# Kernel optimization log

Measured on AMD Instinct MI355X. Metric: run time of the kernel, lower is better.

The kernel has to match this reference:

```python
import jax, jax.numpy as jnp
import numpy as np

LMAX = 2
C1 = 64; C2 = 64; COUT = 64
B = 4096
SUM_RDIM = sum(3**L for L in range(LMAX + 1))   # 13
FEAT1 = C1 * SUM_RDIM                            # 832
FEAT2 = C2 * SUM_RDIM


def _enumerate_paths(Lmax):
    paths = []
    for L1 in range(Lmax + 1):
        for L2 in range(Lmax + 1):
            for k in range(min(L1, L2) + 1):
                Lout = L1 + L2 - 2 * k
                if 0 <= Lout <= Lmax:
                    paths.append((L1, L2, Lout, k, False))
            if L1 >= 1 and L2 >= 1:
                for k in range(min(L1 - 1, L2 - 1) + 1):
                    Lout = L1 + L2 - 2 * k - 1
                    if 0 <= Lout <= Lmax:
                        paths.append((L1, L2, Lout, k, True))
    return paths

PATHS = _enumerate_paths(LMAX)   # 15 paths for Lmax=2


def _path_eq(L1, L2, k, use_eps):
    # Fused equation: W[c,a,b] contracted together with the delta/eps path einsum.
    letters = list('defghijklmnopqrstuvwxyz')  # a,b,c reserved for channels
    i_idx = letters[:L1]
    j_idx = letters[L1:L1 + L2]
    for r in range(k):  # delta: contract last k indices of A with last k of B
        j_idx[L2 - k + r] = i_idx[L1 - k + r]
    i_free = i_idx[:L1 - k]
    j_free = j_idx[:L2 - k]
    eps_sub = None
    if use_eps:  # consume last free index of each side via eps_{p i j}
        p = letters[L1 + L2]
        eps_sub = p + i_free[-1] + j_free[-1]
        i_free, j_free = i_free[:-1], j_free[:-1]
        out = i_free + j_free + [p]
    else:
        out = i_free + j_free
    terms = ['cab', '...a' + ''.join(i_idx), '...b' + ''.join(j_idx)]
    if eps_sub is not None:
        terms.append(eps_sub)
    return ','.join(terms) + '->...c' + ''.join(out)


def _epsilon():
    e = np.zeros((3, 3, 3), dtype=np.float32)
    e[0, 1, 2] = e[1, 2, 0] = e[2, 0, 1] = 1.0
    e[2, 1, 0] = e[1, 0, 2] = e[0, 2, 1] = -1.0
    return jnp.asarray(e)


def _split_by_rank(x, C, Lmax):
    batch = x.shape[:-1]
    out, idx = {}, 0
    for L in range(Lmax + 1):
        d = C * 3**L
        blk = x[..., idx:idx + d]
        idx += d
        out[L] = blk.reshape(*batch, C) if L == 0 else blk.reshape(*batch, C, *((3,) * L))
    return out


def setup_inputs() -> dict:
    key = jax.random.key(0)
    k1, k2, k3 = jax.random.split(key, 3)
    x1 = jax.random.normal(k1, (B, FEAT1), dtype=jnp.float32)
    x2 = jax.random.normal(k2, (B, FEAT2), dtype=jnp.float32)
    weight = jax.random.normal(k3, (len(PATHS) * COUT * C1 * C2,), dtype=jnp.float32) * 0.02
    return {"x1": x1, "x2": x2, "weight": weight}


def reference(x1, x2, weight):
    A = _split_by_rank(x1, C1, LMAX)
    Bt = _split_by_rank(x2, C2, LMAX)
    eps = _epsilon().astype(x1.dtype)
    batch = x1.shape[:-1]
    blocks = {L: jnp.zeros((*batch, COUT) + (3,) * L, dtype=x1.dtype) for L in range(LMAX + 1)}
    wsz = COUT * C1 * C2
    for n, (L1, L2, Lout, k, use_eps) in enumerate(PATHS):
        Wp = weight[n * wsz:(n + 1) * wsz].reshape(COUT, C1, C2)
        eq = _path_eq(L1, L2, k, use_eps)
        ops = (Wp, A[L1], Bt[L2]) + ((eps,) if use_eps else ())
        blocks[Lout] = blocks[Lout] + jnp.einsum(eq, *ops, optimize='optimal')
    parts = [blocks[L].reshape(*batch, COUT * 3**L) for L in range(LMAX + 1)]
    return jnp.concatenate(parts, axis=-1)
```

## Files before the change

kernel.cpp:

```cpp
#include <hip/hip_runtime.h>
#include <cstdint>
#include <cstddef>


#define FEAT 832
#define ZT 64

typedef _Float16 half8 __attribute__((ext_vector_type(8)));
typedef float floatx16 __attribute__((ext_vector_type(16)));

struct Chunk {
  int wbase;
  int o1[3];
  int o2[3];
  float sg[3];
  int d1, d2, nt;
};

__global__ void swz_w_kernel(const float* __restrict__ w, _Float16* __restrict__ o) {
  const int i = blockIdx.x * 256 + threadIdx.x;
  const int lane = i & 63;
  const int pkc  = i >> 6;
  const int cgrp = pkc & 1;
  const int ksg  = (pkc >> 1) & 255;
  const int p    = pkc >> 9;
  const int c  = cgrp * 32 + (lane & 31);
  const int k0 = ksg * 16 + (lane >> 5) * 8;
  const float* src = w + (size_t)p * 262144 + (size_t)c * 4096 + k0;
  const float4 v0 = *(const float4*)(src);
  const float4 v1 = *(const float4*)(src + 4);
  half8 h = { (_Float16)v0.x, (_Float16)v0.y, (_Float16)v0.z, (_Float16)v0.w,
              (_Float16)v1.x, (_Float16)v1.y, (_Float16)v1.z, (_Float16)v1.w };
  *(half8*)(o + (size_t)i * 8) = h;
}

__global__ __launch_bounds__(256) void gather_kernel(
    float* __restrict__ out, const float* __restrict__ part)
{
  __shared__ float T[64][65];
  const int zb = blockIdx.x * 64;
  const int fb = blockIdx.y * 64;
  const int tid = threadIdx.x;
  const int fl = tid >> 6;
  const int zl = tid & 63;
  #pragma unroll
  for (int i = 0; i < 16; ++i) {
    const int f = fb + fl + i * 4;
    int s, c;
    if (f < 64)       { s = 0;              c = f; }
    else if (f < 256) { const int g = f - 64;  c = g / 3; s = 1 + g % 3; }
    else              { const int g = f - 256; c = g / 9; s = 4 + g % 9; }
    T[fl + i * 4][zl] = part[(size_t)s * 262144 + (size_t)c * 4096 + zb + zl];
  }
  __syncthreads();
  const int zr = tid >> 6;
  const int fc = tid & 63;
  #pragma unroll
  for (int i = 0; i < 16; ++i) {
    const int z = zr + i * 4;
    float* o = out + (size_t)(zb + z) * FEAT + fb + fc;
    *o += T[fc][z];
  }
}

__device__ __forceinline__ half8 splat8(_Float16 h) {
  return half8{h, h, h, h, h, h, h, h};
}

template<int NT>
__device__ __forceinline__ void run_chunk(
    const Chunk C, const int zbase, const int zl, const int hf,
    const int lane, const int tid,
    const float* __restrict__ x1, const float* __restrict__ x2,
    const _Float16* __restrict__ Wh, _Float16* __restrict__ XS,
    floatx16& acc0, floatx16& acc1)
{
  __syncthreads();

  #pragma unroll
  for (int t = 0; t < NT; ++t) {
    const size_t base2 = (size_t)zbase * FEAT + C.o2[t];
    for (int e = tid; e < 4096; e += 128) {
      const int zz = e >> 6, b = e & 63;
      XS[(t * 64 + zz) * 72 + b] =
          (_Float16)x2[base2 + (size_t)zz * FEAT + b * C.d2];
    }
  }
  __syncthreads();

  half8 x2r[NT][4];
  #pragma unroll
  for (int t = 0; t < NT; ++t) {
    #pragma unroll
    for (int ks = 0; ks < 4; ++ks)
      x2r[t][ks] = *(const half8*)&XS[(t * 64 + zl) * 72 + ks * 16 + hf * 8];
  }
  __syncthreads();

  #pragma unroll
  for (int t = 0; t < NT; ++t) {
    const float sgf = C.sg[t];
    const int o1 = C.o1[t];
    for (int e = tid; e < 4096; e += 128) {
      const int a = e & 63, zz = e >> 6;
      XS[(t * 64 + a) * 66 + zz] =
          (_Float16)(x1[(size_t)(zbase + zz) * FEAT + o1 + a * C.d1] * sgf);
    }
  }
  __syncthreads();

  const _Float16* __restrict__ Wq = Wh + C.wbase + lane * 8;
  const _Float16* __restrict__ Xq = XS + zl;

  half8 afE[2][4], afO[2][4];
  #pragma unroll
  for (int ks = 0; ks < 4; ++ks) {
    afE[0][ks] = *(const half8*)(Wq + ks * 1024);
    afE[1][ks] = *(const half8*)(Wq + ks * 1024 + 512);
    afO[0][ks] = *(const half8*)(Wq + 4096 + ks * 1024);
    afO[1][ks] = *(const half8*)(Wq + 4096 + ks * 1024 + 512);
  }
  _Float16 sc[NT], scn[NT];
  #pragma unroll
  for (int t = 0; t < NT; ++t) {
    sc[t]  = Xq[(t * 64 + 0) * 66];
    scn[t] = Xq[(t * 64 + 1) * 66];
  }

  #pragma unroll 1
  for (int a = 0; a < 64; a += 2) {
    {
      half8 sv[NT];
      #pragma unroll
      for (int t = 0; t < NT; ++t) sv[t] = splat8(sc[t]);
      if (a + 2 < 64) {
        #pragma unroll
        for (int t = 0; t < NT; ++t) sc[t] = Xq[(t * 64 + a + 2) * 66];
      }
      #pragma unroll
      for (int ks = 0; ks < 4; ++ks) {
        half8 tb = sv[0] * x2r[0][ks];
        if (NT > 1) tb += sv[1] * x2r[1][ks];
        if (NT > 2) tb += sv[2] * x2r[2][ks];
        acc0 = __builtin_amdgcn_mfma_f32_32x32x16_f16(afE[0][ks], tb, acc0, 0, 0, 0);
        acc1 = __builtin_amdgcn_mfma_f32_32x32x16_f16(afE[1][ks], tb, acc1, 0, 0, 0);
      }
      if (a + 2 < 64) {
        const _Float16* wn = Wq + (a + 2) * 4096;
        #pragma unroll
        for (int ks = 0; ks < 4; ++ks) {
          afE[0][ks] = *(const half8*)(wn + ks * 1024);
          afE[1][ks] = *(const half8*)(wn + ks * 1024 + 512);
        }
      }
    }
    {
      half8 sv[NT];
      #pragma unroll
      for (int t = 0; t < NT; ++t) sv[t] = splat8(scn[t]);
      if (a + 3 < 64) {
        #pragma unroll
        for (int t = 0; t < NT; ++t) scn[t] = Xq[(t * 64 + a + 3) * 66];
      }
      #pragma unroll
      for (int ks = 0; ks < 4; ++ks) {
        half8 tb = sv[0] * x2r[0][ks];
        if (NT > 1) tb += sv[1] * x2r[1][ks];
        if (NT > 2) tb += sv[2] * x2r[2][ks];
        acc0 = __builtin_amdgcn_mfma_f32_32x32x16_f16(afO[0][ks], tb, acc0, 0, 0, 0);
        acc1 = __builtin_amdgcn_mfma_f32_32x32x16_f16(afO[1][ks], tb, acc1, 0, 0, 0);
      }
      if (a + 3 < 64) {
        const _Float16* wn = Wq + (a + 3) * 4096;
        #pragma unroll
        for (int ks = 0; ks < 4; ++ks) {
          afO[0][ks] = *(const half8*)(wn + ks * 1024);
          afO[1][ks] = *(const half8*)(wn + ks * 1024 + 512);
        }
      }
    }
  }
}

__global__ __launch_bounds__(128, 2) void tp_kernel(
    const float* __restrict__ x1, const float* __restrict__ x2,
    const _Float16* __restrict__ Wh, float* __restrict__ out,
    float* __restrict__ part)
{
  __shared__ __align__(16) _Float16 XS[3 * 64 * 72];
  __shared__ Chunk chs[7];
  __shared__ int nch_s;

  const int tid  = threadIdx.x;
  const int slot = blockIdx.y;
  const int half = blockIdx.z;
  const int zbase = blockIdx.x * ZT;
  const int zgrp = tid >> 6;
  const int lane = tid & 63;
  const int ln31 = lane & 31;
  const int hf   = lane >> 5;
  const int zl   = zgrp * 32 + ln31;

  int offO, dO, mO;
  if (slot == 0)      { offO = 0;   dO = 1; mO = 0; }
  else if (slot < 4)  { offO = 64;  dO = 3; mO = slot - 1; }
  else                { offO = 256; dO = 9; mO = slot - 4; }

  if (tid == 0) {
    int n = 0;
    auto add = [&](int p, int L1, int L2,
                   int i0, int i1, int i2, int j0, int j1, int j2,
                   float s0, float s1, float s2, int nt) {
      const int offs[3] = {0, 64, 256};
      const int ds[3]   = {1, 3, 9};
      Chunk c;
      c.wbase = p * 262144;
      c.o1[0] = offs[L1] + i0; c.o1[1] = offs[L1] + i1; c.o1[2] = offs[L1] + i2;
      c.o2[0] = offs[L2] + j0; c.o2[1] = offs[L2] + j1; c.o2[2] = offs[L2] + j2;
      c.sg[0] = s0; c.sg[1] = s1; c.sg[2] = s2;
      c.d1 = ds[L1]; c.d2 = ds[L2]; c.nt = nt;
      chs[n++] = c;
    };
    if (slot == 0) {
      add(0, 0,0, 0,0,0, 0,0,0, 1,0,0, 1);
      add(5, 1,1, 0,1,2, 0,1,2, 1,1,1, 3);
      add(13,2,2, 0,1,2, 0,1,2, 1,1,1, 3);
      add(13,2,2, 3,4,5, 3,4,5, 1,1,1, 3);
      add(13,2,2, 6,7,8, 6,7,8, 1,1,1, 3);
    } else if (slot < 4) {
      const int m = slot - 1, p1 = (m+1)%3, p2 = (m+2)%3;
      add(1, 0,1, 0,0,0, m,0,0, 1,0,0, 1);
      add(3, 1,0, m,0,0, 0,0,0, 1,0,0, 1);
      add(6, 1,1, p1,p2,0, p2,p1,0, 1,-1,0, 2);
      add(7, 1,2, 0,1,2, 3*m,3*m+1,3*m+2, 1,1,1, 3);
      add(10,2,1, 3*m,3*m+1,3*m+2, 0,1,2, 1,1,1, 3);
      add(14,2,2, 3*p1,3*p1+1,3*p1+2, 3*p2,3*p2+1,3*p2+2, 1,1,1, 3);
      add(14,2,2, 3*p2,3*p2+1,3*p2+2, 3*p1,3*p1+1,3*p1+2, -1,-1,-1, 3);
    } else {
      const int m = slot - 4, u = m/3, v = m%3, q1 = (v+1)%3, q2 = (v+2)%3;
      add(2, 0,2, 0,0,0, m,0,0, 1,0,0, 1);
      add(4, 1,1, u,0,0, v,0,0, 1,0,0, 1);
      add(8, 1,2, q1,q2,0, 3*u+q2,3*u+q1,0, 1,-1,0, 2);
      add(9, 2,0, m,0,0, 0,0,0, 1,0,0, 1);
      add(11,2,1, 3*u+q1,3*u+q2,0, q2,q1,0, 1,-1,0, 2);
      add(12,2,2, 3*u,3*u+1,3*u+2, 3*v,3*v+1,3*v+2, 1,1,1, 3);
    }
    nch_s = n;
  }
  __syncthreads();
  const int nch = nch_s;

  floatx16 acc0, acc1;
  #pragma unroll
  for (int r = 0; r < 16; ++r) { acc0[r] = 0.0f; acc1[r] = 0.0f; }

  for (int ci = half; ci < nch; ci += 2) {
    const Chunk C = chs[ci];
    if (C.nt == 1)      run_chunk<1>(C, zbase, zl, hf, lane, tid, x1, x2, Wh, XS, acc0, acc1);
    else if (C.nt == 2) run_chunk<2>(C, zbase, zl, hf, lane, tid, x1, x2, Wh, XS, acc0, acc1);
    else                run_chunk<3>(C, zbase, zl, hf, lane, tid, x1, x2, Wh, XS, acc0, acc1);
  }

  if (half == 0) {
    float* __restrict__ op = out + (size_t)(zbase + zl) * FEAT + offO + mO;
    #pragma unroll
    for (int r = 0; r < 16; ++r) {
      const int cr = (r & 3) + 8 * (r >> 2) + 4 * hf;
      op[(size_t)cr * dO]        = acc0[r];
      op[(size_t)(cr + 32) * dO] = acc1[r];
    }
  } else {
    float* __restrict__ op = part + (size_t)slot * 262144 + (zbase + zl);
    #pragma unroll
    for (int r = 0; r < 16; ++r) {
      const int cr = (r & 3) + 8 * (r >> 2) + 4 * hf;
      op[(size_t)cr * 4096]        = acc0[r];
      op[(size_t)(cr + 32) * 4096] = acc1[r];
    }
  }
}

extern "C" void kernel_launch(void* const* d_in, const int* in_sizes, int n_in,
                              void* d_out, int out_size, void* d_ws, size_t ws_size,
                              hipStream_t stream) {
  const float* x1 = (const float*)d_in[0];
  const float* x2 = (const float*)d_in[1];
  const float* w  = (const float*)d_in[2];
  float* out = (float*)d_out;
  _Float16* Wh = (_Float16*)d_ws;
  float* part = (float*)((char*)d_ws + 7864320);

  const int nchunks = 15 * 64 * 4096 / 8;
  hipLaunchKernelGGL(swz_w_kernel, dim3(nchunks / 256), dim3(256), 0, stream, w, Wh);

  dim3 grid(64, 13, 2);
  hipLaunchKernelGGL(tp_kernel, grid, dim3(128), 0, stream, x1, x2, Wh, out, part);

  dim3 ggrid(64, 13);
  hipLaunchKernelGGL(gather_kernel, ggrid, dim3(256), 0, stream, out, part);
}
```

Measured before the change: 381.2 us.

## Split path chunks across up to four z-slices and separate staging buffers

Raises the split-K factor over path chunks from 2 to up to 4 blocks per output tile, sized by the available workspace. Each extra slice writes its own partial plane, and the gather kernel sums them. It also gives x1 and x2 separate shared staging buffers, which removes two barriers per chunk. This adds occupancy and parallelism at the cost of more partial-sum traffic, a heavier gather, and more LDS per block.

```diff
diff --git a/kernel.cpp b/kernel.cpp
--- a/kernel.cpp
+++ b/kernel.cpp
@@ -35,7 +35,7 @@
 }
 
 __global__ __launch_bounds__(256) void gather_kernel(
-    float* __restrict__ out, const float* __restrict__ part)
+    float* __restrict__ out, const float* __restrict__ part, int np)
 {
   __shared__ float T[64][65];
   const int zb = blockIdx.x * 64;
@@ -50,7 +50,11 @@
     if (f < 64)       { s = 0;              c = f; }
     else if (f < 256) { const int g = f - 64;  c = g / 3; s = 1 + g % 3; }
     else              { const int g = f - 256; c = g / 9; s = 4 + g % 9; }
-    T[fl + i * 4][zl] = part[(size_t)s * 262144 + (size_t)c * 4096 + zb + zl];
+    const size_t base = (size_t)s * 262144 + (size_t)c * 4096 + zb + zl;
+    float v = 0.0f;
+    for (int q = 0; q < np; ++q)
+      v += part[(size_t)q * 3407872 + base];
+    T[fl + i * 4][zl] = v;
   }
   __syncthreads();
   const int zr = tid >> 6;
@@ -72,7 +76,8 @@
     const Chunk C, const int zbase, const int zl, const int hf,
     const int lane, const int tid,
     const float* __restrict__ x1, const float* __restrict__ x2,
-    const _Float16* __restrict__ Wh, _Float16* __restrict__ XS,
+    const _Float16* __restrict__ Wh,
+    _Float16* __restrict__ XS2, _Float16* __restrict__ XS1,
     floatx16& acc0, floatx16& acc1)
 {
   __syncthreads();
@@ -82,35 +87,32 @@
     const size_t base2 = (size_t)zbase * FEAT + C.o2[t];
     for (int e = tid; e < 4096; e += 128) {
       const int zz = e >> 6, b = e & 63;
-      XS[(t * 64 + zz) * 72 + b] =
+      XS2[(t * 64 + zz) * 72 + b] =
           (_Float16)x2[base2 + (size_t)zz * FEAT + b * C.d2];
     }
   }
-  __syncthreads();
-
-  half8 x2r[NT][4];
-  #pragma unroll
-  for (int t = 0; t < NT; ++t) {
-    #pragma unroll
-    for (int ks = 0; ks < 4; ++ks)
-      x2r[t][ks] = *(const half8*)&XS[(t * 64 + zl) * 72 + ks * 16 + hf * 8];
-  }
-  __syncthreads();
-
   #pragma unroll
   for (int t = 0; t < NT; ++t) {
     const float sgf = C.sg[t];
     const int o1 = C.o1[t];
     for (int e = tid; e < 4096; e += 128) {
       const int a = e & 63, zz = e >> 6;
-      XS[(t * 64 + a) * 66 + zz] =
+      XS1[(t * 64 + a) * 66 + zz] =
           (_Float16)(x1[(size_t)(zbase + zz) * FEAT + o1 + a * C.d1] * sgf);
     }
   }
   __syncthreads();
 
+  half8 x2r[NT][4];
+  #pragma unroll
+  for (int t = 0; t < NT; ++t) {
+    #pragma unroll
+    for (int ks = 0; ks < 4; ++ks)
+      x2r[t][ks] = *(const half8*)&XS2[(t * 64 + zl) * 72 + ks * 16 + hf * 8];
+  }
+
   const _Float16* __restrict__ Wq = Wh + C.wbase + lane * 8;
-  const _Float16* __restrict__ Xq = XS + zl;
+  const _Float16* __restrict__ Xq = XS1 + zl;
 
   half8 afE[2][4], afO[2][4];
   #pragma unroll
@@ -187,13 +189,15 @@
     const _Float16* __restrict__ Wh, float* __restrict__ out,
     float* __restrict__ part)
 {
-  __shared__ __align__(16) _Float16 XS[3 * 64 * 72];
+  __shared__ __align__(16) _Float16 XS2[3 * 64 * 72];
+  __shared__ __align__(16) _Float16 XS1[3 * 64 * 66];
   __shared__ Chunk chs[7];
   __shared__ int nch_s;
 
   const int tid  = threadIdx.x;
   const int slot = blockIdx.y;
-  const int half = blockIdx.z;
+  const int q    = blockIdx.z;
+  const int nsplit = gridDim.z;
   const int zbase = blockIdx.x * ZT;
   const int zgrp = tid >> 6;
   const int lane = tid & 63;
@@ -254,14 +258,14 @@
   #pragma unroll
   for (int r = 0; r < 16; ++r) { acc0[r] = 0.0f; acc1[r] = 0.0f; }
 
-  for (int ci = half; ci < nch; ci += 2) {
+  for (int ci = q; ci < nch; ci += nsplit) {
     const Chunk C = chs[ci];
-    if (C.nt == 1)      run_chunk<1>(C, zbase, zl, hf, lane, tid, x1, x2, Wh, XS, acc0, acc1);
-    else if (C.nt == 2) run_chunk<2>(C, zbase, zl, hf, lane, tid, x1, x2, Wh, XS, acc0, acc1);
-    else                run_chunk<3>(C, zbase, zl, hf, lane, tid, x1, x2, Wh, XS, acc0, acc1);
-  }
-
-  if (half == 0) {
+    if (C.nt == 1)      run_chunk<1>(C, zbase, zl, hf, lane, tid, x1, x2, Wh, XS2, XS1, acc0, acc1);
+    else if (C.nt == 2) run_chunk<2>(C, zbase, zl, hf, lane, tid, x1, x2, Wh, XS2, XS1, acc0, acc1);
+    else                run_chunk<3>(C, zbase, zl, hf, lane, tid, x1, x2, Wh, XS2, XS1, acc0, acc1);
+  }
+
+  if (q == 0) {
     float* __restrict__ op = out + (size_t)(zbase + zl) * FEAT + offO + mO;
     #pragma unroll
     for (int r = 0; r < 16; ++r) {
@@ -270,7 +274,8 @@
       op[(size_t)(cr + 32) * dO] = acc1[r];
     }
   } else {
-    float* __restrict__ op = part + (size_t)slot * 262144 + (zbase + zl);
+    float* __restrict__ op = part + (size_t)(q - 1) * 3407872
+                                  + (size_t)slot * 262144 + (zbase + zl);
     #pragma unroll
     for (int r = 0; r < 16; ++r) {
       const int cr = (r & 3) + 8 * (r >> 2) + 4 * hf;
@@ -290,12 +295,18 @@
   _Float16* Wh = (_Float16*)d_ws;
   float* part = (float*)((char*)d_ws + 7864320);
 
+  const size_t plane_bytes = 3407872ull * 4ull;
+  int np = (ws_size > 7864320) ? (int)((ws_size - 7864320) / plane_bytes) : 1;
+  if (np > 3) np = 3;
+  if (np < 1) np = 1;
+  const int nsplit = np + 1;
+
   const int nchunks = 15 * 64 * 4096 / 8;
   hipLaunchKernelGGL(swz_w_kernel, dim3(nchunks / 256), dim3(256), 0, stream, w, Wh);
 
-  dim3 grid(64, 13, 2);
+  dim3 grid(64, 13, nsplit);
   hipLaunchKernelGGL(tp_kernel, grid, dim3(128), 0, stream, x1, x2, Wh, out, part);
 
   dim3 ggrid(64, 13);
-  hipLaunchKernelGGL(gather_kernel, ggrid, dim3(256), 0, stream, out, part);
-}
+  hipLaunchKernelGGL(gather_kernel, ggrid, dim3(256), 0, stream, out, part, np);
+}
```

After: 377.1 us. No clear change (-1.1%).
